# Performance work log

Measured on AMD Instinct MI355X. Metric: run time of the kernel, lower is better.

The kernel has to match this reference:

```python
import jax, jax.numpy as jnp
import numpy as np

N = 50000          # number of input points
M = 1024           # num_supernodes
SPACE = 3          # space_dim
FUN = 5            # fun_dim
C = 256            # channel_dim
RADIUS = 0.05      # ball-query radius (pos in unit cube)


def setup_inputs() -> dict:
    key = jax.random.key(0)
    k1, k2, k3, k4, k5 = jax.random.split(key, 5)
    pos = jax.random.uniform(k1, (N, SPACE), jnp.float32)          # unit cube coords
    fun = jax.random.normal(k2, (N, FUN), jnp.float32)             # physical fields
    supernode_idx = jax.random.randint(k3, (M,), 0, N)             # sampled supernodes
    W = jax.random.normal(k4, (C, SPACE + FUN), jnp.float32) / np.sqrt(SPACE + FUN)
    b = jax.random.normal(k5, (C,), jnp.float32) * 0.01
    return {"pos": pos, "fun": fun, "supernode_idx": supernode_idx, "W": W, "b": b}


def reference(pos, fun, supernode_idx, W, b):
    # enc_proj on every point: [N, SPACE+FUN] @ [SPACE+FUN, C] -> [N, C]
    x = jnp.concatenate([pos, fun], axis=-1) @ W.T + b
    # gather supernode positions: [M, SPACE]
    sp = pos[supernode_idx]
    # squared pairwise distances supernode->point: [M, N]
    d2 = jnp.sum((sp[:, None, :] - pos[None, :, :]) ** 2, axis=-1)
    mask = (d2 <= RADIUS * RADIUS).astype(x.dtype)        # radius_graph neighborhood
    cnt = jnp.maximum(mask.sum(axis=-1, keepdims=True), 1.0)
    # mean-aggregate projected point features onto each supernode: [M, C]
    latent = (mask @ x) / cnt
    return latent
```

## Files before the change

### kernel.cpp

```cpp
#include <hip/hip_runtime.h>


#define NC 20
#define NCELLS (NC * NC * NC)
#define SLOTS 64

__global__ __launch_bounds__(256) void sn_scatter(
    const float* __restrict__ pos, const float* __restrict__ fun,
    int* __restrict__ cnt, float* __restrict__ rec, int N)
{
    int i = blockIdx.x * 256 + (int)threadIdx.x;
    if (i >= N) return;
    float px = pos[i * 3 + 0], py = pos[i * 3 + 1], pz = pos[i * 3 + 2];
    int cx = min(NC - 1, (int)(px * (float)NC));
    int cy = min(NC - 1, (int)(py * (float)NC));
    int cz = min(NC - 1, (int)(pz * (float)NC));
    int c = (cz * NC + cy) * NC + cx;
    int k = atomicAdd(cnt + c, 1);
    if (k < SLOTS) {
        float* r = rec + ((size_t)c * SLOTS + k) * 8;
        *(float4*)r       = make_float4(px, py, pz, fun[i * 5 + 0]);
        *(float4*)(r + 4) = make_float4(fun[i * 5 + 1], fun[i * 5 + 2],
                                        fun[i * 5 + 3], fun[i * 5 + 4]);
    }
}

__global__ __launch_bounds__(256) void sn_accum(
    const float* __restrict__ pos, const int* __restrict__ sidx,
    const int* __restrict__ cnt, const float* __restrict__ rec,
    const float* __restrict__ W, const float* __restrict__ bias,
    float* __restrict__ out, int M)
{
    const int lane = (int)threadIdx.x & 63;
    const int m = blockIdx.x * 4 + ((int)threadIdx.x >> 6);
    if (m >= M) return;

    const int idx = sidx[m];
    const float sx = pos[idx * 3 + 0];
    const float sy = pos[idx * 3 + 1];
    const float sz = pos[idx * 3 + 2];

    const float PAD = 0.050001f;
    int cx0 = max(0, (int)floorf((sx - PAD) * (float)NC));
    int cx1 = min(NC - 1, (int)floorf((sx + PAD) * (float)NC));
    int cy0 = max(0, (int)floorf((sy - PAD) * (float)NC));
    int cy1 = min(NC - 1, (int)floorf((sy + PAD) * (float)NC));
    int cz0 = max(0, (int)floorf((sz - PAD) * (float)NC));
    int cz1 = min(NC - 1, (int)floorf((sz + PAD) * (float)NC));
    int nx = cx1 - cx0 + 1, ny = cy1 - cy0 + 1, nz = cz1 - cz0 + 1;
    int ncell = nx * ny * nz;

    int cj = 0, base = 0;
    if (lane < ncell) {
        int jx = lane % nx, jr = lane / nx;
        int jy = jr % ny,   jz = jr / ny;
        int c = ((cz0 + jz) * NC + (cy0 + jy)) * NC + (cx0 + jx);
        cj = min(cnt[c], SLOTS);
        base = c * SLOTS;
    }

    int incl = cj;
#pragma unroll
    for (int d = 1; d < 64; d <<= 1) {
        int v = __shfl_up(incl, d);
        if (lane >= d) incl += v;
    }
    const int excl = incl - cj;
    const int T = __shfl(incl, 63);

    float s0 = 0, s1 = 0, s2 = 0, s3 = 0, s4 = 0, s5 = 0, s6 = 0, s7 = 0, sc = 0;
    const float R2 = 0.0025f;

    for (int t0 = 0; t0 < T; t0 += 64) {
        const int t = t0 + lane;
        const bool act = t < T;
        const int tt = act ? t : 0;
        int lo = 0;
#pragma unroll
        for (int s = 32; s; s >>= 1) {
            int v = __shfl(incl, lo + s - 1);
            if (v <= tt) lo += s;
        }
        const int ridx = __shfl(base, lo) + (tt - __shfl(excl, lo));
        const float* r = rec + (size_t)ridx * 8;
        const float4 a  = *(const float4*)r;
        const float4 b4 = *(const float4*)(r + 4);
        float dx = __fsub_rn(sx, a.x);
        float dy = __fsub_rn(sy, a.y);
        float dz = __fsub_rn(sz, a.z);
        float d2 = __fadd_rn(__fadd_rn(__fmul_rn(dx, dx), __fmul_rn(dy, dy)),
                             __fmul_rn(dz, dz));
        if (act && d2 <= R2) {
            s0 += a.x;  s1 += a.y;  s2 += a.z;  s3 += a.w;
            s4 += b4.x; s5 += b4.y; s6 += b4.z; s7 += b4.w; sc += 1.0f;
        }
    }

#pragma unroll
    for (int d = 32; d; d >>= 1) {
        s0 += __shfl_xor(s0, d); s1 += __shfl_xor(s1, d); s2 += __shfl_xor(s2, d);
        s3 += __shfl_xor(s3, d); s4 += __shfl_xor(s4, d); s5 += __shfl_xor(s5, d);
        s6 += __shfl_xor(s6, d); s7 += __shfl_xor(s7, d); sc += __shfl_xor(sc, d);
    }

    const int c0 = lane * 4;
    float4 o = make_float4(0.f, 0.f, 0.f, 0.f);
    if (sc > 0.0f) {
        const float inv = 1.0f / sc;
        const float f0 = s0 * inv, f1 = s1 * inv, f2 = s2 * inv, f3 = s3 * inv;
        const float f4 = s4 * inv, f5 = s5 * inv, f6 = s6 * inv, f7 = s7 * inv;
        const float4 bb = *(const float4*)(bias + c0);
        float acc[4];
#pragma unroll
        for (int rr = 0; rr < 4; ++rr) {
            const float* w = W + (size_t)(c0 + rr) * 8;
            const float4 w0 = *(const float4*)w;
            const float4 w1 = *(const float4*)(w + 4);
            acc[rr] = f0 * w0.x + f1 * w0.y + f2 * w0.z + f3 * w0.w
                    + f4 * w1.x + f5 * w1.y + f6 * w1.z + f7 * w1.w;
        }
        o = make_float4(bb.x + acc[0], bb.y + acc[1], bb.z + acc[2], bb.w + acc[3]);
    }
    *(float4*)(out + (size_t)m * 256 + c0) = o;
}

extern "C" void kernel_launch(void* const* d_in, const int* in_sizes, int n_in,
                              void* d_out, int out_size, void* d_ws, size_t ws_size,
                              hipStream_t stream) {
    const float* pos  = (const float*)d_in[0];
    const float* fun  = (const float*)d_in[1];
    const int*   sidx = (const int*)d_in[2];
    const float* W    = (const float*)d_in[3];
    const float* b    = (const float*)d_in[4];
    float* out = (float*)d_out;

    const int N = in_sizes[0] / 3;
    const int M = in_sizes[2];

    int*   cnt = (int*)d_ws;
    float* rec = (float*)((char*)d_ws + 32768);

    hipMemsetAsync(cnt, 0, NCELLS * sizeof(int), stream);
    sn_scatter<<<(N + 255) / 256, 256, 0, stream>>>(pos, fun, cnt, rec, N);
    sn_accum<<<(M + 3) / 4, 256, 0, stream>>>(pos, sidx, cnt, rec, W, b, out, M);
}
```

Measured before the change: 72.35 us.

## Fuse memset, scatter and accumulate into one cooperative kernel with grid syncs

Replaces the memset plus two kernel launches with a single cooperative kernel of 256 blocks. Inside it, the cell counters are zeroed, points are binned with a grid-stride loop, and supernodes are accumulated, with grid-wide syncs between the phases. The aim is to remove launch and inter-kernel gaps, which are a large share of a run this short. The cost is two grid barriers and only 256 blocks for the scatter phase, so each thread handles several points. Correctness relies on 256 blocks of 4 supernodes covering M=1024 exactly.

```diff
diff --git a/kernel.cpp b/kernel.cpp
--- a/kernel.cpp
+++ b/kernel.cpp
@@ -1,36 +1,47 @@
 #include <hip/hip_runtime.h>
+#include <hip/hip_cooperative_groups.h>
+
+namespace cg = cooperative_groups;
 
 
 #define NC 20
 #define NCELLS (NC * NC * NC)
 #define SLOTS 64
+#define BLOCKS 256
+#define BLOCK 256
 
-__global__ __launch_bounds__(256) void sn_scatter(
+__global__ __launch_bounds__(BLOCK) void sn_fused(
     const float* __restrict__ pos, const float* __restrict__ fun,
-    int* __restrict__ cnt, float* __restrict__ rec, int N)
+    const int* __restrict__ sidx,
+    const float* __restrict__ W, const float* __restrict__ bias,
+    float* __restrict__ out,
+    int* __restrict__ cnt, float* __restrict__ rec,
+    int N, int M)
 {
-    int i = blockIdx.x * 256 + (int)threadIdx.x;
-    if (i >= N) return;
-    float px = pos[i * 3 + 0], py = pos[i * 3 + 1], pz = pos[i * 3 + 2];
-    int cx = min(NC - 1, (int)(px * (float)NC));
-    int cy = min(NC - 1, (int)(py * (float)NC));
-    int cz = min(NC - 1, (int)(pz * (float)NC));
-    int c = (cz * NC + cy) * NC + cx;
-    int k = atomicAdd(cnt + c, 1);
-    if (k < SLOTS) {
-        float* r = rec + ((size_t)c * SLOTS + k) * 8;
-        *(float4*)r       = make_float4(px, py, pz, fun[i * 5 + 0]);
-        *(float4*)(r + 4) = make_float4(fun[i * 5 + 1], fun[i * 5 + 2],
-                                        fun[i * 5 + 3], fun[i * 5 + 4]);
+    cg::grid_group grid = cg::this_grid();
+    const int tid = blockIdx.x * BLOCK + (int)threadIdx.x;
+
+    for (int c = tid; c < NCELLS; c += BLOCKS * BLOCK) cnt[c] = 0;
+    __threadfence();
+    grid.sync();
+
+    for (int i = tid; i < N; i += BLOCKS * BLOCK) {
+        float px = pos[i * 3 + 0], py = pos[i * 3 + 1], pz = pos[i * 3 + 2];
+        int cx = min(NC - 1, (int)(px * (float)NC));
+        int cy = min(NC - 1, (int)(py * (float)NC));
+        int cz = min(NC - 1, (int)(pz * (float)NC));
+        int c = (cz * NC + cy) * NC + cx;
+        int k = atomicAdd(cnt + c, 1);
+        if (k < SLOTS) {
+            float* r = rec + ((size_t)c * SLOTS + k) * 8;
+            *(float4*)r       = make_float4(px, py, pz, fun[i * 5 + 0]);
+            *(float4*)(r + 4) = make_float4(fun[i * 5 + 1], fun[i * 5 + 2],
+                                            fun[i * 5 + 3], fun[i * 5 + 4]);
+        }
     }
-}
+    __threadfence();
+    grid.sync();
 
-__global__ __launch_bounds__(256) void sn_accum(
-    const float* __restrict__ pos, const int* __restrict__ sidx,
-    const int* __restrict__ cnt, const float* __restrict__ rec,
-    const float* __restrict__ W, const float* __restrict__ bias,
-    float* __restrict__ out, int M)
-{
     const int lane = (int)threadIdx.x & 63;
     const int m = blockIdx.x * 4 + ((int)threadIdx.x >> 6);
     if (m >= M) return;
@@ -134,13 +145,14 @@
     const float* b    = (const float*)d_in[4];
     float* out = (float*)d_out;
 
-    const int N = in_sizes[0] / 3;
-    const int M = in_sizes[2];
+    int N = in_sizes[0] / 3;
+    int M = in_sizes[2];
 
     int*   cnt = (int*)d_ws;
     float* rec = (float*)((char*)d_ws + 32768);
 
-    hipMemsetAsync(cnt, 0, NCELLS * sizeof(int), stream);
-    sn_scatter<<<(N + 255) / 256, 256, 0, stream>>>(pos, fun, cnt, rec, N);
-    sn_accum<<<(M + 3) / 4, 256, 0, stream>>>(pos, sidx, cnt, rec, W, b, out, M);
+    void* args[] = {(void*)&pos, (void*)&fun, (void*)&sidx, (void*)&W, (void*)&b,
+                    (void*)&out, (void*)&cnt, (void*)&rec, (void*)&N, (void*)&M};
+    hipLaunchCooperativeKernel((void*)sn_fused, dim3(BLOCKS), dim3(BLOCK),
+                               args, 0, stream);
 }
```

After: 177.7 us. +145.6%, slower.
